# Performance work log

Measured on AMD Instinct MI355X. Metric: run time of the kernel, lower is better.

## Reference

```python
import jax, jax.numpy as jnp
import numpy as np

# Hair-bundle model parameters (params list)
LAM, LAM_A = 1.0, 10.0          # drag coefficients of bundle / adaptation motor
K_GS, K_SP = 0.75, 0.6          # gating-spring and pivot stiffness
D0, DELTA = 0.5, 0.2            # gating swing and gating sensitivity
F_MAX, S_CA = 1.0, 0.7          # max motor force, Ca feedback strength
C_M, TAU_M = 1.5, 1.0           # motor Ca binding rate / time constant
C_GS, TAU_GS = 1.2, 5.0         # gating-spring Ca binding rate / time constant
C_T, TAU_T = 0.8, 10.0          # transduction Ca binding rate / time constant
HB_NOISE, A_NOISE = 0.05, 0.02  # diffusion amplitudes (constant, used by g)
# force_params
AMP, OMEGA = 0.3, 6.283185307179586

N_SAMPLES = 8_388_608  # ensemble of SDE sample paths
STATE_DIM = 5          # [X, Xa, pm, pgs, pt]


def setup_inputs() -> dict:
    key = jax.random.key(0)
    k_t, k_x = jax.random.split(key)
    t = jax.random.uniform(k_t, (1,), dtype=jnp.float32)
    x = 0.1 * jax.random.normal(k_x, (N_SAMPLES, STATE_DIM), dtype=jnp.float32)
    return {"t": t, "x": x}


def reference(t, x):
    # Fully vectorized drift f(t, x) over the sample axis (replaces the
    # per-sample Python loop + sympy lambda eval in the torch module).
    X, Xa, pm, pgs, pt = x[:, 0], x[:, 1], x[:, 2], x[:, 3], x[:, 4]
    p_open = jax.nn.sigmoid((X - Xa - D0) / DELTA)     # channel open prob
    f_gs = K_GS * (X - Xa - D0 * p_open)               # gating-spring force
    force = AMP * jnp.sin(OMEGA * t[0])                # sin_driving_force(t)
    dX = (-f_gs - K_SP * X) / LAM + force              # force added to var 0 only
    dXa = (f_gs - F_MAX * (1.0 - S_CA * pm)) / LAM_A
    dpm = (C_M * p_open * (1.0 - pm) - pm) / TAU_M
    dpgs = (C_GS * p_open * (1.0 - pgs) - pgs) / TAU_GS
    dpt = (C_T * p_open * (1.0 - pt) - pt) / TAU_T
    return jnp.stack([dX, dXa, dpm, dpgs, dpt], axis=-1)  # [N, 5]
```

## Files before the change

kernel.cpp:

```cpp
#include <hip/hip_runtime.h>


namespace {

constexpr float K_GS      = 0.75f;
constexpr float K_SP      = 0.6f;
constexpr float D0        = 0.5f;
constexpr float DELTA_INV = 5.0f;
constexpr float F_MAX     = 1.0f;
constexpr float S_CA      = 0.7f;
constexpr float LAMA_INV  = 0.1f;
constexpr float AMP       = 0.3f;
constexpr float OMEGA     = 6.283185307179586f;

constexpr int BLOCK       = 256;
constexpr int ROWS_PER_T  = 4;
constexpr int CHUNK_ROWS  = BLOCK * ROWS_PER_T;
constexpr int CHUNK_F4    = CHUNK_ROWS * 5 / 4;

__device__ __forceinline__ void compute_row(float X, float Xa, float pm, float pgs, float pt,
                                            float force, float* o) {
    float d   = X - Xa;
    float z   = (d - D0) * DELTA_INV;
    float p   = 1.0f / (1.0f + __expf(-z));
    float fgs = K_GS * (d - D0 * p);
    o[0] = force - fgs - K_SP * X;
    o[1] = (fgs - (F_MAX - S_CA * pm)) * LAMA_INV;
    o[2] = 1.5f * p * (1.0f - pm) - pm;
    o[3] = (1.2f * p * (1.0f - pgs) - pgs) * 0.2f;
    o[4] = (0.8f * p * (1.0f - pt)  - pt)  * 0.1f;
}

}

__global__ __launch_bounds__(BLOCK) void hb_kernel(
        const float* __restrict__ tp,
        const float* __restrict__ xp,
        float* __restrict__ op,
        long long nrows) {
    __shared__ float4 sIn[CHUNK_F4];
    __shared__ float4 sOut[CHUNK_F4];

    const int tid = threadIdx.x;
    const long long chunk0 = (long long)blockIdx.x * CHUNK_ROWS;

    const float force = AMP * sinf(OMEGA * tp[0]);

    if (chunk0 + CHUNK_ROWS <= nrows) {
        const float4* gsrc = reinterpret_cast<const float4*>(xp + chunk0 * 5);
#pragma unroll
        for (int k = 0; k < 5; ++k)
            sIn[tid + BLOCK * k] = gsrc[tid + BLOCK * k];
        __syncthreads();

        const float4* rsrc = reinterpret_cast<const float4*>(
                                 reinterpret_cast<const float*>(sIn) + tid * 20);
        float vals[20];
#pragma unroll
        for (int k = 0; k < 5; ++k) {
            float4 v = rsrc[k];
            vals[4*k+0] = v.x; vals[4*k+1] = v.y; vals[4*k+2] = v.z; vals[4*k+3] = v.w;
        }

        float res[20];
#pragma unroll
        for (int r = 0; r < ROWS_PER_T; ++r)
            compute_row(vals[5*r+0], vals[5*r+1], vals[5*r+2], vals[5*r+3], vals[5*r+4],
                        force, &res[5*r]);

        float4* rdst = reinterpret_cast<float4*>(
                           reinterpret_cast<float*>(sOut) + tid * 20);
#pragma unroll
        for (int k = 0; k < 5; ++k)
            rdst[k] = make_float4(res[4*k+0], res[4*k+1], res[4*k+2], res[4*k+3]);
        __syncthreads();

        float4* gdst = reinterpret_cast<float4*>(op + chunk0 * 5);
#pragma unroll
        for (int k = 0; k < 5; ++k)
            gdst[tid + BLOCK * k] = sOut[tid + BLOCK * k];
    } else {
        for (long long r = chunk0 + tid * ROWS_PER_T;
             r < nrows && r < chunk0 + (long long)(tid + 1) * ROWS_PER_T; ++r) {
            float in[5], out[5];
            for (int j = 0; j < 5; ++j) in[j] = xp[r*5 + j];
            compute_row(in[0], in[1], in[2], in[3], in[4], force, out);
            for (int j = 0; j < 5; ++j) op[r*5 + j] = out[j];
        }
    }
}

extern "C" void kernel_launch(void* const* d_in, const int* in_sizes, int n_in,
                              void* d_out, int out_size, void* d_ws, size_t ws_size,
                              hipStream_t stream) {
    const float* t = (const float*)d_in[0];
    const float* x = (const float*)d_in[1];
    float* out     = (float*)d_out;

    const long long nrows = (long long)in_sizes[1] / 5;
    const int grid = (int)((nrows + CHUNK_ROWS - 1) / CHUNK_ROWS);

    hb_kernel<<<grid, BLOCK, 0, stream>>>(t, x, out, nrows);
}
```

Before: 283.9 us.

## Use per-wavefront LDS staging with wave barriers and nontemporal global access

Each 64-lane wavefront now stages its own slice of rows through a single shared buffer. This replaces the block-wide __syncthreads with wave barriers and halves LDS use by reusing the same buffer for input and output. Global loads and stores become nontemporal to avoid cache pollution on this streaming workload. The risk is that wave_barrier alone may not order the LDS writes and reads across lanes without an explicit waitcnt, although the compiler normally inserts one.

```diff
diff --git a/kernel.cpp b/kernel.cpp
--- a/kernel.cpp
+++ b/kernel.cpp
@@ -2,6 +2,8 @@
 
 
 namespace {
+
+typedef float f32x4 __attribute__((ext_vector_type(4)));
 
 constexpr float K_GS      = 0.75f;
 constexpr float K_SP      = 0.6f;
@@ -17,6 +19,7 @@
 constexpr int ROWS_PER_T  = 4;
 constexpr int CHUNK_ROWS  = BLOCK * ROWS_PER_T;
 constexpr int CHUNK_F4    = CHUNK_ROWS * 5 / 4;
+constexpr int WAVE_F4     = 64 * ROWS_PER_T * 5 / 4;
 
 __device__ __forceinline__ void compute_row(float X, float Xa, float pm, float pgs, float pt,
                                             float force, float* o) {
@@ -38,47 +41,50 @@
         const float* __restrict__ xp,
         float* __restrict__ op,
         long long nrows) {
-    __shared__ float4 sIn[CHUNK_F4];
-    __shared__ float4 sOut[CHUNK_F4];
+    __shared__ f32x4 s[CHUNK_F4];
 
-    const int tid = threadIdx.x;
+    const int tid   = threadIdx.x;
+    const int lane  = tid & 63;
+    const int wbase = (tid >> 6) * WAVE_F4;
+
     const long long chunk0 = (long long)blockIdx.x * CHUNK_ROWS;
 
     const float force = AMP * sinf(OMEGA * tp[0]);
 
     if (chunk0 + CHUNK_ROWS <= nrows) {
-        const float4* gsrc = reinterpret_cast<const float4*>(xp + chunk0 * 5);
+        const f32x4* gsrc = reinterpret_cast<const f32x4*>(xp + chunk0 * 5) + wbase;
+        f32x4*       gdst = reinterpret_cast<f32x4*>(op + chunk0 * 5)       + wbase;
+        f32x4*       sw   = s + wbase;
+
 #pragma unroll
         for (int k = 0; k < 5; ++k)
-            sIn[tid + BLOCK * k] = gsrc[tid + BLOCK * k];
-        __syncthreads();
+            sw[64 * k + lane] = __builtin_nontemporal_load(gsrc + 64 * k + lane);
 
-        const float4* rsrc = reinterpret_cast<const float4*>(
-                                 reinterpret_cast<const float*>(sIn) + tid * 20);
+        __builtin_amdgcn_wave_barrier();
+
+        f32x4* r4 = reinterpret_cast<f32x4*>(reinterpret_cast<float*>(sw) + lane * 20);
+
         float vals[20];
 #pragma unroll
         for (int k = 0; k < 5; ++k) {
-            float4 v = rsrc[k];
+            f32x4 v = r4[k];
             vals[4*k+0] = v.x; vals[4*k+1] = v.y; vals[4*k+2] = v.z; vals[4*k+3] = v.w;
         }
 
-        float res[20];
 #pragma unroll
         for (int r = 0; r < ROWS_PER_T; ++r)
             compute_row(vals[5*r+0], vals[5*r+1], vals[5*r+2], vals[5*r+3], vals[5*r+4],
-                        force, &res[5*r]);
+                        force, &vals[5*r]);
 
-        float4* rdst = reinterpret_cast<float4*>(
-                           reinterpret_cast<float*>(sOut) + tid * 20);
 #pragma unroll
         for (int k = 0; k < 5; ++k)
-            rdst[k] = make_float4(res[4*k+0], res[4*k+1], res[4*k+2], res[4*k+3]);
-        __syncthreads();
+            r4[k] = (f32x4){vals[4*k+0], vals[4*k+1], vals[4*k+2], vals[4*k+3]};
 
-        float4* gdst = reinterpret_cast<float4*>(op + chunk0 * 5);
+        __builtin_amdgcn_wave_barrier();
+
 #pragma unroll
         for (int k = 0; k < 5; ++k)
-            gdst[tid + BLOCK * k] = sOut[tid + BLOCK * k];
+            __builtin_nontemporal_store(sw[64 * k + lane], gdst + 64 * k + lane);
     } else {
         for (long long r = chunk0 + tid * ROWS_PER_T;
              r < nrows && r < chunk0 + (long long)(tid + 1) * ROWS_PER_T; ++r) {
```

Result: faster. 270.4 us (-4.8%).
